# Performance work log

Hardware: AMD Instinct MI355X
Metric: run time of the kernel (lower is better)

## Reference

```python
import jax, jax.numpy as jnp
import numpy as np

CUTOFF = 8.0
NUM_G = 50
HID = 128
NUM_INTER = 3
NUM_NODES = 50000
NUM_EDGES = 1600000
NUM_GRAPHS = 128
MAX_Z = 100
LOG2 = float(np.log(2.0))


def ssp(x):
    # PyG ShiftedSoftplus
    return jax.nn.softplus(x) - LOG2


def setup_inputs() -> dict:
    key = jax.random.key(0)
    ks = jax.random.split(key, 20)
    s = 0.1
    pos = jax.random.normal(ks[0], (NUM_NODES, 3), dtype=jnp.float32) * 4.0
    edge_shift = jax.random.normal(ks[1], (NUM_EDGES, 3), dtype=jnp.float32) * 0.5
    z = jax.random.randint(ks[2], (NUM_NODES,), 0, MAX_Z, dtype=jnp.int32)
    edge_index = jax.random.randint(ks[3], (2, NUM_EDGES), 0, NUM_NODES, dtype=jnp.int32)
    batch = jnp.sort(jax.random.randint(ks[4], (NUM_NODES,), 0, NUM_GRAPHS, dtype=jnp.int32))
    emb = jax.random.normal(ks[5], (MAX_Z, HID), dtype=jnp.float32) * s
    mlp_w1 = jax.random.normal(ks[6], (NUM_INTER, NUM_G, HID), dtype=jnp.float32) * s
    mlp_b1 = jnp.zeros((NUM_INTER, HID), jnp.float32)
    mlp_w2 = jax.random.normal(ks[7], (NUM_INTER, HID, HID), dtype=jnp.float32) * s
    mlp_b2 = jnp.zeros((NUM_INTER, HID), jnp.float32)
    cf_w1 = jax.random.normal(ks[8], (NUM_INTER, HID, HID), dtype=jnp.float32) * s  # no bias (PyG lin1)
    cf_w2 = jax.random.normal(ks[9], (NUM_INTER, HID, HID), dtype=jnp.float32) * s
    cf_b2 = jnp.zeros((NUM_INTER, HID), jnp.float32)
    lin_w = jax.random.normal(ks[10], (NUM_INTER, HID, HID), dtype=jnp.float32) * s
    lin_b = jnp.zeros((NUM_INTER, HID), jnp.float32)
    head_w1 = jax.random.normal(ks[11], (HID, HID // 2), dtype=jnp.float32) * s
    head_b1 = jnp.zeros((HID // 2,), jnp.float32)
    head_w2 = jax.random.normal(ks[12], (HID // 2, 1), dtype=jnp.float32) * s
    head_b2 = jnp.zeros((1,), jnp.float32)
    return dict(pos=pos, edge_shift=edge_shift, emb=emb, mlp_w1=mlp_w1, mlp_b1=mlp_b1,
                mlp_w2=mlp_w2, mlp_b2=mlp_b2, cf_w1=cf_w1, cf_w2=cf_w2, cf_b2=cf_b2,
                lin_w=lin_w, lin_b=lin_b, head_w1=head_w1, head_b1=head_b1,
                head_w2=head_w2, head_b2=head_b2, z=z, edge_index=edge_index, batch=batch)


def reference(pos, edge_shift, emb, mlp_w1, mlp_b1, mlp_w2, mlp_b2, cf_w1, cf_w2, cf_b2,
              lin_w, lin_b, head_w1, head_b1, head_w2, head_b2, z, edge_index, batch):
    src, dst = edge_index[0], edge_index[1]
    # edge distances: pos[row] - (pos[col] + shift)
    rel = pos[src] - (pos[dst] + edge_shift)            # [E,3]
    w = jnp.linalg.norm(rel, axis=-1)                   # [E]
    # Gaussian smearing
    offset = jnp.linspace(0.0, CUTOFF, NUM_G, dtype=pos.dtype)
    coeff = -0.5 / (offset[1] - offset[0]) ** 2
    edge_attr = jnp.exp(coeff * (w[:, None] - offset) ** 2)   # [E,50]
    # cosine cutoff
    C = 0.5 * (jnp.cos(w * jnp.pi / CUTOFF) + 1.0)            # [E]
    h = emb[z]                                                # [N,128]
    for i in range(NUM_INTER):
        Wf = (ssp(edge_attr @ mlp_w1[i] + mlp_b1[i]) @ mlp_w2[i] + mlp_b2[i]) * C[:, None]  # [E,128]
        msg = (h @ cf_w1[i])[src] * Wf                   # gather-multiply  [E,128]
        agg = jax.ops.segment_sum(msg, dst, num_segments=NUM_NODES)         # scatter-sum [N,128]
        h = h + (ssp(agg @ cf_w2[i] + cf_b2[i]) @ lin_w[i] + lin_b[i])
    out_atom = ssp(h @ head_w1 + head_b1) @ head_w2 + head_b2               # [N,1]
    sums = jax.ops.segment_sum(out_atom, batch, num_segments=NUM_GRAPHS)    # [G,1]
    counts = jax.ops.segment_sum(jnp.ones((NUM_NODES, 1), out_atom.dtype), batch, num_segments=NUM_GRAPHS)
    return sums / jnp.maximum(counts, 1.0)  # mean readout; out_proj is Identity (128==128)
```

## Files before the change

### kernel.cpp

```cpp
#include <hip/hip_runtime.h>
#include <hip/hip_fp16.h>
#include <math.h>

#define NNODES  50000
#define NEDGES  1600000
#define NGRAPHS 128
#define HID     128
#define NG      50
#define NITER   3
#define TPTS    2048
#define WMAX    12.0f
#define PI_F    3.14159265358979323846f

typedef __attribute__((ext_vector_type(4))) _Float16 half4;
typedef __attribute__((ext_vector_type(4))) float   f32x4;

__device__ __forceinline__ float ssp(float x) {
    float sp = fmaxf(x, 0.0f) + log1pf(expf(-fabsf(x)));
    return sp - 0.69314718055994530942f;
}

__global__ __launch_bounds__(256) void k_init_h(const float* __restrict__ emb,
                                                const int* __restrict__ z,
                                                float* __restrict__ h,
                                                _Float16* __restrict__ hH)
{
    int idx = blockIdx.x * 256 + threadIdx.x;
    int n = idx >> 7, c = idx & 127;
    float v = emb[(z[n] << 7) + c];
    h[idx] = v;
    hH[idx] = (_Float16)v;
}

__global__ __launch_bounds__(128) void k_wt(const float* __restrict__ in,
                                            _Float16* __restrict__ out)
{
    int it = blockIdx.x >> 7, c = blockIdx.x & 127, j = threadIdx.x;
    out[(size_t)it * 16384 + c * 128 + j] = (_Float16)in[(size_t)it * 16384 + j * 128 + c];
}

__global__ __launch_bounds__(128) void k_table(const float* __restrict__ W1,
                                               const float* __restrict__ B1,
                                               const float* __restrict__ W2,
                                               const float* __restrict__ B2,
                                               __half* __restrict__ ti)
{
    int it = blockIdx.x / TPTS;
    int pt = blockIdx.x - it * TPTS;
    const float* W1i = W1 + (size_t)it * NG * HID;
    const float* B1i = B1 + (size_t)it * HID;
    const float* W2i = W2 + (size_t)it * HID * HID;
    const float* B2i = B2 + (size_t)it * HID;

    const float step = WMAX / (float)(TPTS - 1);
    float w0 = pt * step;
    int ptn = (pt < TPTS - 1) ? pt + 1 : pt;
    float w1v = ptn * step;

    __shared__ float sEA[2][NG];
    __shared__ float sT1[2][HID];
    int k = threadIdx.x;
    {
        float dx = 8.0f / 49.0f;
        float coeff = -0.5f / (dx * dx);
        if (k < NG) {
            float diff = w0 - (float)k * dx;
            sEA[0][k] = expf(coeff * diff * diff);
        } else if (k >= 64 && k < 64 + NG) {
            float diff = w1v - (float)(k - 64) * dx;
            sEA[1][k - 64] = expf(coeff * diff * diff);
        }
    }
    __syncthreads();
    float a0 = B1i[k], a1 = a0;
    for (int g = 0; g < NG; ++g) {
        float wv = W1i[g * HID + k];
        a0 = fmaf(sEA[0][g], wv, a0);
        a1 = fmaf(sEA[1][g], wv, a1);
    }
    sT1[0][k] = ssp(a0);
    sT1[1][k] = ssp(a1);
    __syncthreads();
    float b0 = B2i[k], b1v = b0;
    for (int j = 0; j < HID; ++j) {
        float wv = W2i[j * HID + k];
        b0  = fmaf(sT1[0][j], wv, b0);
        b1v = fmaf(sT1[1][j], wv, b1v);
    }
    size_t base = ((size_t)it * TPTS + pt) * 256;
    int pair = k >> 1, within = k & 1;
    ti[base + pair * 4 + within]     = __float2half(b0);
    ti[base + pair * 4 + within + 2] = __float2half(b1v - b0);
}

__global__ __launch_bounds__(256) void k_hist(const int* __restrict__ ei,
                                              int* __restrict__ deg)
{
    int e = blockIdx.x * 256 + threadIdx.x;
    if (e >= NEDGES) return;
    atomicAdd(&deg[ei[NEDGES + e]], 1);
}

#define SCAN_T 1024
#define CHUNK  49
__global__ __launch_bounds__(SCAN_T) void k_scan(const int* __restrict__ deg,
                                                 int* __restrict__ rowptr,
                                                 int* __restrict__ cursor)
{
    int tid = threadIdx.x;
    int base = tid * CHUNK;
    int vals[CHUNK];
    int local = 0;
    #pragma unroll
    for (int i = 0; i < CHUNK; ++i) {
        int idx = base + i;
        int v = (idx < NNODES) ? deg[idx] : 0;
        vals[i] = local;
        local += v;
    }
    int lane = tid & 63, wid = tid >> 6;
    int x = local;
    #pragma unroll
    for (int off = 1; off < 64; off <<= 1) {
        int y = __shfl_up(x, off);
        if (lane >= off) x += y;
    }
    __shared__ int wsum[16];
    __shared__ int woff[17];
    if (lane == 63) wsum[wid] = x;
    __syncthreads();
    if (tid == 0) {
        int acc = 0;
        #pragma unroll
        for (int i = 0; i < 16; ++i) { woff[i] = acc; acc += wsum[i]; }
        woff[16] = acc;
    }
    __syncthreads();
    int threadExcl = woff[wid] + x - local;
    #pragma unroll
    for (int i = 0; i < CHUNK; ++i) {
        int idx = base + i;
        if (idx < NNODES) {
            int p = threadExcl + vals[i];
            rowptr[idx] = p;
            cursor[idx] = p;
        }
    }
    if (tid == SCAN_T - 1) rowptr[NNODES] = woff[16];
}

__global__ __launch_bounds__(256) void k_scatter(const int* __restrict__ ei,
                                                 const float* __restrict__ pos,
                                                 const float* __restrict__ shift,
                                                 int* __restrict__ cursor,
                                                 uint4* __restrict__ rec)
{
    int e = blockIdx.x * 256 + threadIdx.x;
    if (e >= NEDGES) return;
    int s = ei[e], d = ei[NEDGES + e];
    float rx = pos[3*s+0] - (pos[3*d+0] + shift[3*e+0]);
    float ry = pos[3*s+1] - (pos[3*d+1] + shift[3*e+1]);
    float rz = pos[3*s+2] - (pos[3*d+2] + shift[3*e+2]);
    float w = sqrtf(rx*rx + ry*ry + rz*rz);
    const float SCALE = (float)(TPTS - 1) / WMAX;
    float t = fminf(w * SCALE, (float)(TPTS - 1));
    int i0 = (int)t; if (i0 > TPTS - 2) i0 = TPTS - 2;
    float fr = t - (float)i0;
    float C = 0.5f * (cosf(w * (PI_F / 8.0f)) + 1.0f);
    __half2 fr2 = __float2half2_rn(fr);
    __half2 c2  = __float2half2_rn(C);
    int slot = atomicAdd(&cursor[d], 1);
    rec[slot] = make_uint4((unsigned)(s * 256), (unsigned)(i0 * 512),
                           *(unsigned*)&fr2, *(unsigned*)&c2);
}

__device__ __forceinline__ void edge_contrib(uint4 rv,
                                             const char* __restrict__ hfLane,
                                             const char* __restrict__ tbLane,
                                             float& ax, float& ay)
{
    int srcB = __builtin_amdgcn_readfirstlane((int)rv.x);
    int tblO = __builtin_amdgcn_readfirstlane((int)rv.y);
    int fru  = __builtin_amdgcn_readfirstlane((int)rv.z);
    int cu   = __builtin_amdgcn_readfirstlane((int)rv.w);
    __half2 fr2 = *reinterpret_cast<__half2*>(&fru);
    __half2 c2  = *reinterpret_cast<__half2*>(&cu);
    uint2 tv = *reinterpret_cast<const uint2*>(tbLane + tblO);
    __half2 hv = *reinterpret_cast<const __half2*>(hfLane + srcB);
    __half2 vals = *reinterpret_cast<__half2*>(&tv.x);
    __half2 dels = *reinterpret_cast<__half2*>(&tv.y);
    __half2 f2 = __hfma2(fr2, dels, vals);
    __half2 ch = __hmul2(c2, hv);
    ax = fmaf(__low2float(f2),  __low2float(ch),  ax);
    ay = fmaf(__high2float(f2), __high2float(ch), ay);
}

__global__ __launch_bounds__(256) void k_gather(const uint4* __restrict__ rec,
                                                const int* __restrict__ rowptr,
                                                const __half* __restrict__ hfH,
                                                const __half* __restrict__ tableH,
                                                __half2* __restrict__ aggH)
{
    int node = blockIdx.x * 4 + (threadIdx.x >> 6);
    int lane = threadIdx.x & 63;
    const char* hfLane = (const char*)hfH + lane * 4;
    const char* tbLane = (const char*)tableH + lane * 8;
    int beg = rowptr[node], end = rowptr[node + 1];
    float ax0 = 0.f, ay0 = 0.f, ax1 = 0.f, ay1 = 0.f;
    int k = beg;
    for (; k + 4 <= end; k += 4) {
        uint4 r0 = rec[k], r1 = rec[k+1], r2 = rec[k+2], r3 = rec[k+3];
        edge_contrib(r0, hfLane, tbLane, ax0, ay0);
        edge_contrib(r1, hfLane, tbLane, ax1, ay1);
        edge_contrib(r2, hfLane, tbLane, ax0, ay0);
        edge_contrib(r3, hfLane, tbLane, ax1, ay1);
    }
    for (; k < end; ++k) edge_contrib(rec[k], hfLane, tbLane, ax0, ay0);
    aggH[(size_t)node * 64 + lane] = __floats2half2_rn(ax0 + ax1, ay0 + ay1);
}

__global__ __launch_bounds__(256) void k_ngemm_mfma(const _Float16* __restrict__ hH,
                                                    const _Float16* __restrict__ Wt,
                                                    _Float16* __restrict__ outH)
{
    int tid = threadIdx.x;
    int wave = tid >> 6, l = tid & 63;
    int lr = l & 15, lg = l >> 4;
    int r0 = blockIdx.x * 64 + wave * 16;
    f32x4 acc[8];
    #pragma unroll
    for (int ct = 0; ct < 8; ++ct) acc[ct] = (f32x4){0.f, 0.f, 0.f, 0.f};
    const _Float16* aRow = hH + (size_t)(r0 + lr) * HID;
    #pragma unroll
    for (int kk = 0; kk < 8; ++kk) {
        half4 a = *(const half4*)(aRow + kk * 16 + lg * 4);
        #pragma unroll
        for (int ct = 0; ct < 8; ++ct) {
            half4 b = *(const half4*)(Wt + (size_t)(ct * 16 + lr) * HID + kk * 16 + lg * 4);
            acc[ct] = __builtin_amdgcn_mfma_f32_16x16x16f16(a, b, acc[ct], 0, 0, 0);
        }
    }
    #pragma unroll
    for (int ct = 0; ct < 8; ++ct) {
        #pragma unroll
        for (int r = 0; r < 4; ++r) {
            int row = r0 + lg * 4 + r;
            if (row < NNODES) outH[(size_t)row * HID + ct * 16 + lr] = (_Float16)acc[ct][r];
        }
    }
}

__global__ __launch_bounds__(256) void k_update_mfma(const _Float16* __restrict__ aggH,
                                                     const _Float16* __restrict__ W2t,
                                                     const float* __restrict__ B2,
                                                     const _Float16* __restrict__ Lt,
                                                     const float* __restrict__ LB,
                                                     float* __restrict__ h,
                                                     _Float16* __restrict__ hH,
                                                     const _Float16* __restrict__ W1n,
                                                     _Float16* __restrict__ hfOut)
{
    __shared__ _Float16 sT[64 * 128];
    int tid = threadIdx.x;
    int wave = tid >> 6, l = tid & 63;
    int lr = l & 15, lg = l >> 4;
    int r0 = blockIdx.x * 64 + wave * 16;

    f32x4 acc[8];
    #pragma unroll
    for (int ct = 0; ct < 8; ++ct) acc[ct] = (f32x4){0.f, 0.f, 0.f, 0.f};
    const _Float16* aRow = aggH + (size_t)(r0 + lr) * HID;
    #pragma unroll
    for (int kk = 0; kk < 8; ++kk) {
        half4 a = *(const half4*)(aRow + kk * 16 + lg * 4);
        #pragma unroll
        for (int ct = 0; ct < 8; ++ct) {
            half4 b = *(const half4*)(W2t + (size_t)(ct * 16 + lr) * HID + kk * 16 + lg * 4);
            acc[ct] = __builtin_amdgcn_mfma_f32_16x16x16f16(a, b, acc[ct], 0, 0, 0);
        }
    }
    #pragma unroll
    for (int ct = 0; ct < 8; ++ct) {
        #pragma unroll
        for (int r = 0; r < 4; ++r) {
            int rl = wave * 16 + lg * 4 + r;
            int col = ct * 16 + lr;
            float v = ssp(acc[ct][r] + B2[col]);
            int byte = rl * 256 + col * 2;
            byte ^= (rl & 7) << 4;
            *(_Float16*)((char*)sT + byte) = (_Float16)v;
        }
    }
    __syncthreads();
    f32x4 acc2[8];
    #pragma unroll
    for (int ct = 0; ct < 8; ++ct) acc2[ct] = (f32x4){0.f, 0.f, 0.f, 0.f};
    int rl2 = wave * 16 + lr;
    #pragma unroll
    for (int kk = 0; kk < 8; ++kk) {
        int byte = rl2 * 256 + (kk * 16 + lg * 4) * 2;
        byte ^= (rl2 & 7) << 4;
        half4 a = *(const half4*)((char*)sT + byte);
        #pragma unroll
        for (int ct = 0; ct < 8; ++ct) {
            half4 b = *(const half4*)(Lt + (size_t)(ct * 16 + lr) * HID + kk * 16 + lg * 4);
            acc2[ct] = __builtin_amdgcn_mfma_f32_16x16x16f16(a, b, acc2[ct], 0, 0, 0);
        }
    }
    __syncthreads();
    #pragma unroll
    for (int ct = 0; ct < 8; ++ct) {
        #pragma unroll
        for (int r = 0; r < 4; ++r) {
            int row = r0 + lg * 4 + r;
            int col = ct * 16 + lr;
            float hv = 0.f;
            if (row < NNODES) {
                hv = h[(size_t)row * HID + col] + acc2[ct][r] + LB[col];
                h[(size_t)row * HID + col] = hv;
                hH[(size_t)row * HID + col] = (_Float16)hv;
            }
            if (W1n) {
                int rl = wave * 16 + lg * 4 + r;
                int byte = rl * 256 + col * 2;
                byte ^= (rl & 7) << 4;
                *(_Float16*)((char*)sT + byte) = (_Float16)hv;
            }
        }
    }
    if (W1n) {
        __syncthreads();
        f32x4 acc3[8];
        #pragma unroll
        for (int ct = 0; ct < 8; ++ct) acc3[ct] = (f32x4){0.f, 0.f, 0.f, 0.f};
        #pragma unroll
        for (int kk = 0; kk < 8; ++kk) {
            int byte = rl2 * 256 + (kk * 16 + lg * 4) * 2;
            byte ^= (rl2 & 7) << 4;
            half4 a = *(const half4*)((char*)sT + byte);
            #pragma unroll
            for (int ct = 0; ct < 8; ++ct) {
                half4 b = *(const half4*)(W1n + (size_t)(ct * 16 + lr) * HID + kk * 16 + lg * 4);
                acc3[ct] = __builtin_amdgcn_mfma_f32_16x16x16f16(a, b, acc3[ct], 0, 0, 0);
            }
        }
        #pragma unroll
        for (int ct = 0; ct < 8; ++ct) {
            #pragma unroll
            for (int r = 0; r < 4; ++r) {
                int row = r0 + lg * 4 + r;
                if (row < NNODES) hfOut[(size_t)row * HID + ct * 16 + lr] = (_Float16)acc3[ct][r];
            }
        }
    }
}

__global__ __launch_bounds__(512) void k_head(const float* __restrict__ h,
                                              const float* __restrict__ w1,
                                              const float* __restrict__ b1,
                                              const float* __restrict__ w2,
                                              const float* __restrict__ b2,
                                              const int* __restrict__ batch,
                                              float* __restrict__ sums_pad)
{
    __shared__ float sA[128 * 132];
    int r0 = blockIdx.x * 128;
    int tid = threadIdx.x;
    for (int idx = tid; idx < 128 * 32; idx += 512) {
        int r = idx >> 5, c4 = idx & 31;
        int row = r0 + r;
        float4 v = make_float4(0.f, 0.f, 0.f, 0.f);
        if (row < NNODES) v = *(const float4*)(h + (size_t)row * HID + c4 * 4);
        *(float4*)(&sA[r * 132 + c4 * 4]) = v;
    }
    __syncthreads();
    int tx = tid & 7, ty = tid >> 3;
    int cc = tx * 8, ee = ty * 2;
    float acc[2][8];
    {
        float4 b0 = *(const float4*)(b1 + cc);
        float4 bb = *(const float4*)(b1 + cc + 4);
        #pragma unroll
        for (int e = 0; e < 2; ++e) {
            acc[e][0]=b0.x; acc[e][1]=b0.y; acc[e][2]=b0.z; acc[e][3]=b0.w;
            acc[e][4]=bb.x; acc[e][5]=bb.y; acc[e][6]=bb.z; acc[e][7]=bb.w;
        }
    }
    #pragma unroll 4
    for (int j = 0; j < HID; ++j) {
        float a0 = sA[(ee + 0) * 132 + j];
        float a1 = sA[(ee + 1) * 132 + j];
        float4 w0 = *(const float4*)(w1 + (size_t)j * 64 + cc);
        float4 wv1 = *(const float4*)(w1 + (size_t)j * 64 + cc + 4);
        float wv[8] = {w0.x,w0.y,w0.z,w0.w,wv1.x,wv1.y,wv1.z,wv1.w};
        #pragma unroll
        for (int c = 0; c < 8; ++c) {
            acc[0][c] = fmaf(a0, wv[c], acc[0][c]);
            acc[1][c] = fmaf(a1, wv[c], acc[1][c]);
        }
    }
    float4 w2a = *(const float4*)(w2 + cc);
    float4 w2b = *(const float4*)(w2 + cc + 4);
    float w2v[8] = {w2a.x,w2a.y,w2a.z,w2a.w,w2b.x,w2b.y,w2b.z,w2b.w};
    float bias2 = b2[0];
    #pragma unroll
    for (int e = 0; e < 2; ++e) {
        float part = 0.f;
        #pragma unroll
        for (int c = 0; c < 8; ++c) part = fmaf(ssp(acc[e][c]), w2v[c], part);
        part += __shfl_down(part, 4, 8);
        part += __shfl_down(part, 2, 8);
        part += __shfl_down(part, 1, 8);
        if (tx == 0) {
            int row = r0 + ee + e;
            if (row < NNODES) {
                int b = batch[row];
                atomicAdd(&sums_pad[b * 16], part + bias2);
            }
        }
    }
}

__global__ void k_final(const float* __restrict__ sums_pad,
                        const int* __restrict__ batch,
                        float* __restrict__ out)
{
    int g = threadIdx.x;
    if (g >= NGRAPHS) return;
    int lo = 0, hi = NNODES;
    while (lo < hi) { int mid = (lo + hi) >> 1; if (batch[mid] < g) lo = mid + 1; else hi = mid; }
    int a = lo;
    lo = 0; hi = NNODES;
    while (lo < hi) { int mid = (lo + hi) >> 1; if (batch[mid] < g + 1) lo = mid + 1; else hi = mid; }
    float cnt = (float)(lo - a);
    out[g] = sums_pad[g * 16] / fmaxf(cnt, 1.0f);
}

extern "C" void kernel_launch(void* const* d_in, const int* in_sizes, int n_in,
                              void* d_out, int out_size, void* d_ws, size_t ws_size,
                              hipStream_t stream)
{
    const float* pos     = (const float*)d_in[0];
    const float* shift   = (const float*)d_in[1];
    const float* emb     = (const float*)d_in[2];
    const float* mlp_w1  = (const float*)d_in[3];
    const float* mlp_b1  = (const float*)d_in[4];
    const float* mlp_w2  = (const float*)d_in[5];
    const float* mlp_b2  = (const float*)d_in[6];
    const float* cf_w1   = (const float*)d_in[7];
    const float* cf_w2   = (const float*)d_in[8];
    const float* cf_b2   = (const float*)d_in[9];
    const float* lin_w   = (const float*)d_in[10];
    const float* lin_b   = (const float*)d_in[11];
    const float* head_w1 = (const float*)d_in[12];
    const float* head_b1 = (const float*)d_in[13];
    const float* head_w2 = (const float*)d_in[14];
    const float* head_b2 = (const float*)d_in[15];
    const int*   z       = (const int*)d_in[16];
    const int*   ei      = (const int*)d_in[17];
    const int*   batch   = (const int*)d_in[18];
    float* out = (float*)d_out;

    float* ws = (float*)d_ws;
    size_t off = 0;
    float*    h       = ws + off; off += (size_t)NNODES * HID;
    _Float16* hH      = (_Float16*)(ws + off); off += (size_t)(NNODES + 64) * HID / 2;
    _Float16* hfH     = (_Float16*)(ws + off); off += (size_t)(NNODES + 64) * HID / 2;
    _Float16* aggH    = (_Float16*)(ws + off); off += (size_t)(NNODES + 64) * HID / 2;
    __half*   tableH  = (__half*)(ws + off); off += (size_t)3 * TPTS * 256 / 2;
    _Float16* w1t     = (_Float16*)(ws + off); off += (size_t)3 * HID * HID / 2;
    _Float16* w2t     = (_Float16*)(ws + off); off += (size_t)3 * HID * HID / 2;
    _Float16* lwt     = (_Float16*)(ws + off); off += (size_t)3 * HID * HID / 2;
    uint4*    rec     = (uint4*)(ws + off); off += (size_t)4 * NEDGES;
    int*      rowptr  = (int*)(ws + off); off += NNODES + 1;
    int*      deg     = (int*)(ws + off); off += NNODES;
    int*      cursor  = (int*)(ws + off); off += NNODES;
    float*    sums_pad= ws + off; off += NGRAPHS * 16;

    hipMemsetAsync(deg, 0, NNODES * sizeof(int), stream);
    hipMemsetAsync(sums_pad, 0, NGRAPHS * 16 * sizeof(float), stream);

    k_hist<<<(NEDGES + 255) / 256, 256, 0, stream>>>(ei, deg);
    k_scan<<<1, SCAN_T, 0, stream>>>(deg, rowptr, cursor);
    k_scatter<<<(NEDGES + 255) / 256, 256, 0, stream>>>(ei, pos, shift, cursor, rec);

    k_init_h<<<NNODES * HID / 256, 256, 0, stream>>>(emb, z, h, hH);
    k_table<<<3 * TPTS, 128, 0, stream>>>(mlp_w1, mlp_b1, mlp_w2, mlp_b2, tableH);
    k_wt<<<3 * 128, 128, 0, stream>>>(cf_w1, w1t);
    k_wt<<<3 * 128, 128, 0, stream>>>(cf_w2, w2t);
    k_wt<<<3 * 128, 128, 0, stream>>>(lin_w, lwt);

    int gblk = (NNODES + 63) / 64;
    k_ngemm_mfma<<<gblk, 256, 0, stream>>>(hH, w1t, hfH);
    for (int i = 0; i < NITER; ++i) {
        k_gather<<<NNODES / 4, 256, 0, stream>>>(rec, rowptr, (const __half*)hfH,
                                                 tableH + (size_t)i * TPTS * 256,
                                                 (__half2*)aggH);
        k_update_mfma<<<gblk, 256, 0, stream>>>(aggH, w2t + (size_t)i * HID * HID,
                                                cf_b2 + (size_t)i * HID,
                                                lwt + (size_t)i * HID * HID,
                                                lin_b + (size_t)i * HID, h, hH,
                                                (i < NITER - 1) ? w1t + (size_t)(i + 1) * HID * HID : nullptr,
                                                hfH);
    }
    k_head<<<(NNODES + 127) / 128, 512, 0, stream>>>(h, head_w1, head_b1, head_w2, head_b2, batch, sums_pad);
    k_final<<<1, 128, 0, stream>>>(sums_pad, batch, out);
}
```

Before: 1.170 ms.

## Split node GEMMs across waves by column tiles and unfuse next-layer projection

The node GEMM and update kernels now give each 256-thread block 16 rows instead of 64. The four waves split the 128 output columns, two 16-wide tiles each, so each wave keeps 2 accumulators instead of 8. This launches four times as many blocks and lowers register pressure, which should raise occupancy. The fused next-layer h@cf_w1 projection inside the update kernel is removed and k_ngemm_mfma is launched at the start of each iteration instead. That costs an extra kernel launch and an extra read of hH per layer. The row bounds checks are dropped, which relies on NNODES being divisible by 16.

```diff
diff --git a/kernel.cpp b/kernel.cpp
--- a/kernel.cpp
+++ b/kernel.cpp
@@ -226,27 +226,27 @@
     int tid = threadIdx.x;
     int wave = tid >> 6, l = tid & 63;
     int lr = l & 15, lg = l >> 4;
-    int r0 = blockIdx.x * 64 + wave * 16;
-    f32x4 acc[8];
-    #pragma unroll
-    for (int ct = 0; ct < 8; ++ct) acc[ct] = (f32x4){0.f, 0.f, 0.f, 0.f};
+    int r0 = blockIdx.x * 16;
+    f32x4 acc[2];
+    acc[0] = (f32x4){0.f, 0.f, 0.f, 0.f};
+    acc[1] = (f32x4){0.f, 0.f, 0.f, 0.f};
     const _Float16* aRow = hH + (size_t)(r0 + lr) * HID;
     #pragma unroll
     for (int kk = 0; kk < 8; ++kk) {
         half4 a = *(const half4*)(aRow + kk * 16 + lg * 4);
         #pragma unroll
-        for (int ct = 0; ct < 8; ++ct) {
+        for (int c = 0; c < 2; ++c) {
+            int ct = wave * 2 + c;
             half4 b = *(const half4*)(Wt + (size_t)(ct * 16 + lr) * HID + kk * 16 + lg * 4);
-            acc[ct] = __builtin_amdgcn_mfma_f32_16x16x16f16(a, b, acc[ct], 0, 0, 0);
-        }
-    }
-    #pragma unroll
-    for (int ct = 0; ct < 8; ++ct) {
-        #pragma unroll
-        for (int r = 0; r < 4; ++r) {
-            int row = r0 + lg * 4 + r;
-            if (row < NNODES) outH[(size_t)row * HID + ct * 16 + lr] = (_Float16)acc[ct][r];
-        }
+            acc[c] = __builtin_amdgcn_mfma_f32_16x16x16f16(a, b, acc[c], 0, 0, 0);
+        }
+    }
+    #pragma unroll
+    for (int c = 0; c < 2; ++c) {
+        int col = (wave * 2 + c) * 16 + lr;
+        #pragma unroll
+        for (int r = 0; r < 4; ++r)
+            outH[(size_t)(r0 + lg * 4 + r) * HID + col] = (_Float16)acc[c][r];
     }
 }
 
@@ -256,101 +256,67 @@
                                                      const _Float16* __restrict__ Lt,
                                                      const float* __restrict__ LB,
                                                      float* __restrict__ h,
-                                                     _Float16* __restrict__ hH,
-                                                     const _Float16* __restrict__ W1n,
-                                                     _Float16* __restrict__ hfOut)
-{
-    __shared__ _Float16 sT[64 * 128];
+                                                     _Float16* __restrict__ hH)
+{
+    __shared__ _Float16 sT[16 * 128];
     int tid = threadIdx.x;
     int wave = tid >> 6, l = tid & 63;
     int lr = l & 15, lg = l >> 4;
-    int r0 = blockIdx.x * 64 + wave * 16;
-
-    f32x4 acc[8];
-    #pragma unroll
-    for (int ct = 0; ct < 8; ++ct) acc[ct] = (f32x4){0.f, 0.f, 0.f, 0.f};
+    int r0 = blockIdx.x * 16;
+
+    f32x4 acc[2];
+    acc[0] = (f32x4){0.f, 0.f, 0.f, 0.f};
+    acc[1] = (f32x4){0.f, 0.f, 0.f, 0.f};
     const _Float16* aRow = aggH + (size_t)(r0 + lr) * HID;
     #pragma unroll
     for (int kk = 0; kk < 8; ++kk) {
         half4 a = *(const half4*)(aRow + kk * 16 + lg * 4);
         #pragma unroll
-        for (int ct = 0; ct < 8; ++ct) {
+        for (int c = 0; c < 2; ++c) {
+            int ct = wave * 2 + c;
             half4 b = *(const half4*)(W2t + (size_t)(ct * 16 + lr) * HID + kk * 16 + lg * 4);
-            acc[ct] = __builtin_amdgcn_mfma_f32_16x16x16f16(a, b, acc[ct], 0, 0, 0);
-        }
-    }
-    #pragma unroll
-    for (int ct = 0; ct < 8; ++ct) {
+            acc[c] = __builtin_amdgcn_mfma_f32_16x16x16f16(a, b, acc[c], 0, 0, 0);
+        }
+    }
+    #pragma unroll
+    for (int c = 0; c < 2; ++c) {
+        int col = (wave * 2 + c) * 16 + lr;
+        float bias = B2[col];
         #pragma unroll
         for (int r = 0; r < 4; ++r) {
-            int rl = wave * 16 + lg * 4 + r;
-            int col = ct * 16 + lr;
-            float v = ssp(acc[ct][r] + B2[col]);
+            int rl = lg * 4 + r;
+            float v = ssp(acc[c][r] + bias);
             int byte = rl * 256 + col * 2;
             byte ^= (rl & 7) << 4;
             *(_Float16*)((char*)sT + byte) = (_Float16)v;
         }
     }
     __syncthreads();
-    f32x4 acc2[8];
-    #pragma unroll
-    for (int ct = 0; ct < 8; ++ct) acc2[ct] = (f32x4){0.f, 0.f, 0.f, 0.f};
-    int rl2 = wave * 16 + lr;
+    f32x4 acc2[2];
+    acc2[0] = (f32x4){0.f, 0.f, 0.f, 0.f};
+    acc2[1] = (f32x4){0.f, 0.f, 0.f, 0.f};
     #pragma unroll
     for (int kk = 0; kk < 8; ++kk) {
-        int byte = rl2 * 256 + (kk * 16 + lg * 4) * 2;
-        byte ^= (rl2 & 7) << 4;
+        int byte = lr * 256 + (kk * 16 + lg * 4) * 2;
+        byte ^= (lr & 7) << 4;
         half4 a = *(const half4*)((char*)sT + byte);
         #pragma unroll
-        for (int ct = 0; ct < 8; ++ct) {
+        for (int c = 0; c < 2; ++c) {
+            int ct = wave * 2 + c;
             half4 b = *(const half4*)(Lt + (size_t)(ct * 16 + lr) * HID + kk * 16 + lg * 4);
-            acc2[ct] = __builtin_amdgcn_mfma_f32_16x16x16f16(a, b, acc2[ct], 0, 0, 0);
-        }
-    }
-    __syncthreads();
-    #pragma unroll
-    for (int ct = 0; ct < 8; ++ct) {
+            acc2[c] = __builtin_amdgcn_mfma_f32_16x16x16f16(a, b, acc2[c], 0, 0, 0);
+        }
+    }
+    #pragma unroll
+    for (int c = 0; c < 2; ++c) {
+        int col = (wave * 2 + c) * 16 + lr;
+        float lb = LB[col];
         #pragma unroll
         for (int r = 0; r < 4; ++r) {
             int row = r0 + lg * 4 + r;
-            int col = ct * 16 + lr;
-            float hv = 0.f;
-            if (row < NNODES) {
-                hv = h[(size_t)row * HID + col] + acc2[ct][r] + LB[col];
-                h[(size_t)row * HID + col] = hv;
-                hH[(size_t)row * HID + col] = (_Float16)hv;
-            }
-            if (W1n) {
-                int rl = wave * 16 + lg * 4 + r;
-                int byte = rl * 256 + col * 2;
-                byte ^= (rl & 7) << 4;
-                *(_Float16*)((char*)sT + byte) = (_Float16)hv;
-            }
-        }
-    }
-    if (W1n) {
-        __syncthreads();
-        f32x4 acc3[8];
-        #pragma unroll
-        for (int ct = 0; ct < 8; ++ct) acc3[ct] = (f32x4){0.f, 0.f, 0.f, 0.f};
-        #pragma unroll
-        for (int kk = 0; kk < 8; ++kk) {
-            int byte = rl2 * 256 + (kk * 16 + lg * 4) * 2;
-            byte ^= (rl2 & 7) << 4;
-            half4 a = *(const half4*)((char*)sT + byte);
-            #pragma unroll
-            for (int ct = 0; ct < 8; ++ct) {
-                half4 b = *(const half4*)(W1n + (size_t)(ct * 16 + lr) * HID + kk * 16 + lg * 4);
-                acc3[ct] = __builtin_amdgcn_mfma_f32_16x16x16f16(a, b, acc3[ct], 0, 0, 0);
-            }
-        }
-        #pragma unroll
-        for (int ct = 0; ct < 8; ++ct) {
-            #pragma unroll
-            for (int r = 0; r < 4; ++r) {
-                int row = r0 + lg * 4 + r;
-                if (row < NNODES) hfOut[(size_t)row * HID + ct * 16 + lr] = (_Float16)acc3[ct][r];
-            }
+            float hv = h[(size_t)row * HID + col] + acc2[c][r] + lb;
+            h[(size_t)row * HID + col] = hv;
+            hH[(size_t)row * HID + col] = (_Float16)hv;
         }
     }
 }
@@ -490,18 +456,16 @@
     k_wt<<<3 * 128, 128, 0, stream>>>(cf_w2, w2t);
     k_wt<<<3 * 128, 128, 0, stream>>>(lin_w, lwt);
 
-    int gblk = (NNODES + 63) / 64;
-    k_ngemm_mfma<<<gblk, 256, 0, stream>>>(hH, w1t, hfH);
+    int gblk = NNODES / 16;
     for (int i = 0; i < NITER; ++i) {
+        k_ngemm_mfma<<<gblk, 256, 0, stream>>>(hH, w1t + (size_t)i * HID * HID, hfH);
         k_gather<<<NNODES / 4, 256, 0, stream>>>(rec, rowptr, (const __half*)hfH,
                                                  tableH + (size_t)i * TPTS * 256,
                                                  (__half2*)aggH);
         k_update_mfma<<<gblk, 256, 0, stream>>>(aggH, w2t + (size_t)i * HID * HID,
                                                 cf_b2 + (size_t)i * HID,
                                                 lwt + (size_t)i * HID * HID,
-                                                lin_b + (size_t)i * HID, h, hH,
-                                                (i < NITER - 1) ? w1t + (size_t)(i + 1) * HID * HID : nullptr,
-                                                hfH);
+                                                lin_b + (size_t)i * HID, h, hH);
     }
     k_head<<<(NNODES + 127) / 128, 512, 0, stream>>>(h, head_w1, head_b1, head_w2, head_b2, batch, sums_pad);
     k_final<<<1, 128, 0, stream>>>(sums_pad, batch, out);
```

Measured after the change: 1.101 ms. 1.06x faster.
